# Performance work log

Hardware: AMD Instinct MI355X
Metric: run time of the kernel (lower is better)

The kernel has to match this reference:

```python
import jax, jax.numpy as jnp
import numpy as np

B, T, S0 = 8, 4, 4096
D_MODEL, H, D, R, RANK = 2048, 16, 128, 64, 512
C = D - R  # content dim = 64


def _rope(x, positions):
    # x: [B, H, T, R]; rotate-half style RoPE as in the torch module
    half = x.shape[-1] // 2
    inv_freq = 1.0 / (10000.0 ** (jnp.arange(half, dtype=jnp.float32) / half))
    freqs = positions.astype(jnp.float32)[:, None] * inv_freq[None, :]  # [T, half]
    cos = jnp.cos(freqs)[None, None].astype(x.dtype)
    sin = jnp.sin(freqs)[None, None].astype(x.dtype)
    x1, x2 = x[..., :half], x[..., half:]
    return jnp.concatenate([x1 * cos - x2 * sin, x1 * sin + x2 * cos], axis=-1)


def setup_inputs() -> dict:
    key = jax.random.key(0)
    ks = jax.random.split(key, 9)
    s = 0.02
    return {
        "x": jax.random.normal(ks[0], (B, T, D_MODEL), jnp.float32),
        "cache_c_kv": jax.random.normal(ks[1], (B, S0, RANK), jnp.float32),
        "cache_k_rope": jax.random.normal(ks[2], (B, S0, H, R), jnp.float32),
        "w_q": jax.random.normal(ks[3], (D_MODEL, H * C), jnp.float32) * s,
        "w_q_rope": jax.random.normal(ks[4], (D_MODEL, H * R), jnp.float32) * s,
        "w_kv_down": jax.random.normal(ks[5], (D_MODEL, RANK), jnp.float32) * s,
        "w_kv_up": jax.random.normal(ks[6], (RANK, H * D), jnp.float32) * s,
        "w_k_rope": jax.random.normal(ks[7], (D_MODEL, H * R), jnp.float32) * s,
        "w_out": jax.random.normal(ks[8], (H * D, D_MODEL), jnp.float32) * s,
    }


def reference(x, cache_c_kv, cache_k_rope, w_q, w_q_rope, w_kv_down, w_kv_up, w_k_rope, w_out):
    cache_len = cache_c_kv.shape[1]
    positions = jnp.arange(cache_len, cache_len + T)

    # queries
    q_content = (x @ w_q).reshape(B, T, H, C).transpose(0, 2, 1, 3)        # [B,H,T,C]
    q_rope = (x @ w_q_rope).reshape(B, T, H, R).transpose(0, 2, 1, 3)      # [B,H,T,R]
    q_rope = _rope(q_rope, positions)
    q = jnp.concatenate([q_content, q_rope], axis=-1)                       # [B,H,T,D]

    # new compressed kv + rope keys, append to cache
    c_kv_new = x @ w_kv_down                                                # [B,T,RANK]
    k_rope_new = (x @ w_k_rope).reshape(B, T, H, R).transpose(0, 2, 1, 3)
    k_rope_new = _rope(k_rope_new, positions).transpose(0, 2, 1, 3)         # [B,T,H,R]
    c_kv = jnp.concatenate([cache_c_kv, c_kv_new], axis=1)                  # [B,S,RANK]
    k_rope = jnp.concatenate([cache_k_rope, k_rope_new], axis=1)            # [B,S,H,R]

    # decompress full cache every step (the expensive MLA pattern)
    S = c_kv.shape[1]
    kv = (c_kv @ w_kv_up).reshape(B, S, H, D)                               # [B,S,H,D]
    k_content = kv[..., :C].transpose(0, 2, 1, 3)                           # [B,H,S,C]
    v = kv.transpose(0, 2, 1, 3)                                            # [B,H,S,D]
    k = jnp.concatenate([k_content, k_rope.transpose(0, 2, 1, 3)], axis=-1) # [B,H,S,D]

    # kv_cache present => is_prefill False => no causal mask (faithful to source)
    scale = 1.0 / jnp.sqrt(jnp.asarray(D, dtype=q.dtype))
    scores = jnp.einsum('bhtd,bhsd->bhts', q, k) * scale
    attn = jax.nn.softmax(scores, axis=-1)
    out = jnp.einsum('bhts,bhsd->bhtd', attn, v)                            # [B,H,T,D]
    out = out.transpose(0, 2, 1, 3).reshape(B, T, H * D)
    return out @ w_out                                                       # [B,T,D_MODEL]
```

## Files before the change

kernel.cpp:

```cpp
#include <hip/hip_runtime.h>
#include <hip/hip_fp16.h>
#include <cmath>

#define BB 8
#define TT 4
#define HH 16
#define DDIM 128
#define RRDIM 64
#define CCDIM 64
#define RANKC 512
#define DMODEL 2048
#define S0C 4096
#define NQ 64
#define HD 2048
#define NACT 3584
#define NSC 65
#define NG 17
#define SPAD 4160
#define SCALE_ATT 0.08838834764831845f
#define LP 72

typedef __attribute__((ext_vector_type(8))) short bf16x8;
typedef __attribute__((ext_vector_type(4))) float f32x4;
typedef unsigned short ushortT;

#define AIDX(row, kk) ((row)*132 + (((row)>>2)<<2) + (kk))

static __device__ __forceinline__ unsigned short f2bf(float x) {
  unsigned u = __float_as_uint(x);
  u += 0x7FFFu + ((u >> 16) & 1u);
  return (unsigned short)(u >> 16);
}
static __device__ __forceinline__ float bf2f(unsigned v16) {
  return __uint_as_float(v16 << 16);
}
static __device__ __forceinline__ unsigned pk2(float a, float b) {
  return (unsigned)f2bf(a) | ((unsigned)f2bf(b) << 16);
}

__global__ __launch_bounds__(256) void k_front(const float* __restrict__ A,
                                               const float* __restrict__ w0,
                                               const float* __restrict__ w1,
                                               const float* __restrict__ w2,
                                               const float* __restrict__ w3,
                                               const float* __restrict__ cckv,
                                               float* __restrict__ part,
                                               ushortT* __restrict__ ckvT) {
  __shared__ float shf[4352];
  const int tid = threadIdx.x;
  const int bx = blockIdx.x;
  if (bx < 448) {
    const int cb = bx % 28;
    const int k0 = (bx / 28) * 128;
    const float* W; int N, lc0, off;
    if (cb < 8)       { W = w0; N = 1024; lc0 = cb * 128;        off = 0; }
    else if (cb < 16) { W = w1; N = 1024; lc0 = (cb - 8) * 128;  off = 1024; }
    else if (cb < 20) { W = w2; N = 512;  lc0 = (cb - 16) * 128; off = 2048; }
    else              { W = w3; N = 1024; lc0 = (cb - 20) * 128; off = 2560; }
    {
      const int row = tid >> 3;
      const int kseg = (tid & 7) * 16;
      const float4* s4 = reinterpret_cast<const float4*>(A + (size_t)row * DMODEL + k0 + kseg);
      float4 v0 = s4[0], v1 = s4[1], v2 = s4[2], v3 = s4[3];
      *reinterpret_cast<float4*>(&shf[AIDX(row, kseg)])      = v0;
      *reinterpret_cast<float4*>(&shf[AIDX(row, kseg + 4)])  = v1;
      *reinterpret_cast<float4*>(&shf[AIDX(row, kseg + 8)])  = v2;
      *reinterpret_cast<float4*>(&shf[AIDX(row, kseg + 12)]) = v3;
    }
    __syncthreads();
    const int cg = tid & 31;
    const int rg = tid >> 5;
    float acc[4][4];
    #pragma unroll
    for (int r = 0; r < 4; ++r)
      #pragma unroll
      for (int c = 0; c < 4; ++c) acc[r][c] = 0.f;
    #pragma unroll 4
    for (int kk = 0; kk < 128; ++kk) {
      const float4 w4 = *reinterpret_cast<const float4*>(W + (size_t)(k0 + kk) * N + lc0 + cg * 4);
      const float wv[4] = {w4.x, w4.y, w4.z, w4.w};
      #pragma unroll
      for (int r = 0; r < 4; ++r) {
        const float av = shf[AIDX(rg * 4 + r, kk)];
        #pragma unroll
        for (int c = 0; c < 4; ++c) acc[r][c] = fmaf(av, wv[c], acc[r][c]);
      }
    }
    #pragma unroll
    for (int r = 0; r < 4; ++r) {
      float4 o = make_float4(acc[r][0], acc[r][1], acc[r][2], acc[r][3]);
      *reinterpret_cast<float4*>(part + ((size_t)(bx / 28) * 32 + rg * 4 + r) * NACT + off + lc0 + cg * 4) = o;
    }
  } else if (bx < 960) {
    ushortT* tlds = reinterpret_cast<ushortT*>(shf);
    const int idx = bx - 448;
    const int b = idx >> 6, c = idx & 63;
    const float* src = cckv + ((size_t)b * S0C + c * 64) * RANKC;
    ushortT* dstT = ckvT + ((size_t)(b * NSC + c) * RANKC) * 64;
    const int s = tid >> 2, rq = tid & 3;
    const int rloc = tid >> 1, shalf = (tid & 1) * 32;
    for (int slab = 0; slab < 4; ++slab) {
      const int r0 = slab * 128;
      #pragma unroll
      for (int i = 0; i < 8; ++i) {
        const float4 v = *reinterpret_cast<const float4*>(src + (size_t)s * RANKC + r0 + rq * 32 + i * 4);
        *reinterpret_cast<uint2*>(&tlds[s * 136 + rq * 32 + i * 4]) =
            make_uint2(pk2(v.x, v.y), pk2(v.z, v.w));
      }
      __syncthreads();
      unsigned wv[16];
      #pragma unroll
      for (int k = 0; k < 16; ++k) {
        const unsigned t0 = tlds[(shalf + 2 * k)     * 136 + rloc];
        const unsigned t1 = tlds[(shalf + 2 * k + 1) * 136 + rloc];
        wv[k] = t0 | (t1 << 16);
      }
      uint4* d = reinterpret_cast<uint4*>(dstT + ((size_t)(r0 + rloc)) * 64 + shalf);
      d[0] = make_uint4(wv[0], wv[1], wv[2], wv[3]);
      d[1] = make_uint4(wv[4], wv[5], wv[6], wv[7]);
      d[2] = make_uint4(wv[8], wv[9], wv[10], wv[11]);
      d[3] = make_uint4(wv[12], wv[13], wv[14], wv[15]);
      __syncthreads();
    }
  } else {
    const int b = bx - 960;
    uint4* p = reinterpret_cast<uint4*>(ckvT + ((size_t)(b * NSC + 64) * RANKC) * 64);
    const uint4 z = make_uint4(0, 0, 0, 0);
    for (int i = tid; i < 4096; i += 256) p[i] = z;
  }
}

__global__ __launch_bounds__(256) void k_proj(const float* __restrict__ A,
                                              const float* __restrict__ W,
                                              float* __restrict__ part,
                                              int N, int NTOT, int coloff) {
  __shared__ float a_lds[4352];
  const int tid = threadIdx.x;
  const int c0 = blockIdx.x * 128;
  const int k0 = blockIdx.y * 128;
  {
    const int row = tid >> 3;
    const int kseg = (tid & 7) * 16;
    const float4* s4 = reinterpret_cast<const float4*>(A + (size_t)row * DMODEL + k0 + kseg);
    float4 v0 = s4[0], v1 = s4[1], v2 = s4[2], v3 = s4[3];
    *reinterpret_cast<float4*>(&a_lds[AIDX(row, kseg)])      = v0;
    *reinterpret_cast<float4*>(&a_lds[AIDX(row, kseg + 4)])  = v1;
    *reinterpret_cast<float4*>(&a_lds[AIDX(row, kseg + 8)])  = v2;
    *reinterpret_cast<float4*>(&a_lds[AIDX(row, kseg + 12)]) = v3;
  }
  __syncthreads();
  const int cg = tid & 31;
  const int rg = tid >> 5;
  float acc[4][4];
  #pragma unroll
  for (int r = 0; r < 4; ++r)
    #pragma unroll
    for (int c = 0; c < 4; ++c) acc[r][c] = 0.f;
  #pragma unroll 4
  for (int kk = 0; kk < 128; ++kk) {
    const float4 w4 = *reinterpret_cast<const float4*>(W + (size_t)(k0 + kk) * N + c0 + cg * 4);
    const float wv[4] = {w4.x, w4.y, w4.z, w4.w};
    #pragma unroll
    for (int r = 0; r < 4; ++r) {
      const float av = a_lds[AIDX(rg * 4 + r, kk)];
      #pragma unroll
      for (int c = 0; c < 4; ++c) acc[r][c] = fmaf(av, wv[c], acc[r][c]);
    }
  }
  #pragma unroll
  for (int r = 0; r < 4; ++r) {
    float4 o = make_float4(acc[r][0], acc[r][1], acc[r][2], acc[r][3]);
    *reinterpret_cast<float4*>(part + ((size_t)blockIdx.y * 32 + rg * 4 + r) * NTOT + coloff + c0 + cg * 4) = o;
  }
}

__global__ __launch_bounds__(256) void k_reduce(const float* __restrict__ part,
                                                float* __restrict__ out, int total, int nsplit) {
  int g = blockIdx.x * 256 + threadIdx.x;
  if (g >= total) return;
  float s = 0.f;
  #pragma unroll 4
  for (int c = 0; c < nsplit; ++c) s += part[(size_t)c * total + g];
  out[g] = s;
}

__global__ __launch_bounds__(256) void k_qlatrope(const float* __restrict__ act,
                                                  const float* __restrict__ wup,
                                                  ushortT* __restrict__ qlat,
                                                  float* __restrict__ qrope,
                                                  float* __restrict__ ckvn,
                                                  float* __restrict__ krn,
                                                  ushortT* __restrict__ ckvT) {
  __shared__ float wt[64 * 132];
  __shared__ float a_s[32 * 68];
  const int tid = threadIdx.x;
  const int bx = blockIdx.x;
  if (bx < 64) {
    const int h = bx & 15;
    const int r0 = (bx >> 4) * 128;
    {
      const int r = tid >> 1;
      const int cseg = (tid & 1) * 32;
      const float* src = wup + (size_t)(r0 + r) * HD + h * DDIM + cseg;
      #pragma unroll
      for (int u = 0; u < 8; ++u) {
        const float4 v = *reinterpret_cast<const float4*>(src + u * 4);
        wt[(cseg + u * 4 + 0) * 132 + r] = v.x;
        wt[(cseg + u * 4 + 1) * 132 + r] = v.y;
        wt[(cseg + u * 4 + 2) * 132 + r] = v.z;
        wt[(cseg + u * 4 + 3) * 132 + r] = v.w;
      }
    }
    {
      const int bt = tid >> 3;
      const int cseg = (tid & 7) * 8;
      const float4* s4 = reinterpret_cast<const float4*>(act + (size_t)bt * NACT + h * CCDIM + cseg);
      float4 v0 = s4[0], v1 = s4[1];
      *reinterpret_cast<float4*>(&a_s[bt * 68 + cseg])     = v0;
      *reinterpret_cast<float4*>(&a_s[bt * 68 + cseg + 4]) = v1;
    }
    __syncthreads();
    const int r = tid & 127;
    const int bth = tid >> 7;
    float acc[16];
    #pragma unroll
    for (int i = 0; i < 16; ++i) acc[i] = 0.f;
    #pragma unroll 8
    for (int c = 0; c < 64; ++c) {
      const float wv = wt[c * 132 + r];
      #pragma unroll
      for (int i = 0; i < 16; ++i)
        acc[i] = fmaf(a_s[(bth * 16 + i) * 68 + c], wv, acc[i]);
    }
    #pragma unroll
    for (int i = 0; i < 16; ++i) {
      const int bt = bth * 16 + i;
      const int b = bt >> 2, t = bt & 3;
      qlat[((size_t)(b * NQ) + h * TT + t) * RANKC + r0 + r] = f2bf(acc[i]);
    }
    return;
  }
  int g = (bx - 64) * 256 + tid;
  if (g < BB * TT * HH * 32) {
    const int hj = g & 31;
    const int h = (g >> 5) & 15;
    const int t = (g >> 9) & 3;
    const int b = g >> 11;
    const float* arow = act + (size_t)(b * TT + t) * NACT + 1024 + h * RRDIM;
    const float x1 = arow[hj], x2 = arow[hj + 32];
    const double fr = (double)(S0C + t) * pow(10000.0, -(double)hj / 32.0);
    const float cs = (float)cos(fr), sn = (float)sin(fr);
    const int qi = h * TT + t;
    qrope[((size_t)b * NQ + qi) * RRDIM + hj]      = x1 * cs - x2 * sn;
    qrope[((size_t)b * NQ + qi) * RRDIM + hj + 32] = x1 * sn + x2 * cs;
    return;
  }
  g -= BB * TT * HH * 32;
  if (g < BB * TT * HH * 32) {
    const int hj = g & 31;
    const int h = (g >> 5) & 15;
    const int t = (g >> 9) & 3;
    const int b = g >> 11;
    const float* arow = act + (size_t)(b * TT + t) * NACT + 2560 + h * RRDIM;
    const float x1 = arow[hj], x2 = arow[hj + 32];
    const double fr = (double)(S0C + t) * pow(10000.0, -(double)hj / 32.0);
    const float cs = (float)cos(fr), sn = (float)sin(fr);
    krn[((size_t)(b * TT + t) * HH + h) * RRDIM + hj]      = x1 * cs - x2 * sn;
    krn[((size_t)(b * TT + t) * HH + h) * RRDIM + hj + 32] = x1 * sn + x2 * cs;
    return;
  }
  g -= BB * TT * HH * 32;
  if (g < BB * TT * RANKC) {
    const int r = g & 511;
    const int bt = g >> 9;
    const int b = bt >> 2, t = bt & 3;
    const float v = act[(size_t)bt * NACT + 2048 + r];
    ckvn[g] = v;
    ckvT[(((size_t)(b * NSC + 64) * RANKC) + r) * 64 + t] = f2bf(v);
  }
}

__global__ __launch_bounds__(256) void k_rscore(const float* __restrict__ cache_kr,
                                                const float* __restrict__ krn,
                                                const float* __restrict__ qrope,
                                                __half* __restrict__ rs) {
  const int bh = blockIdx.x;
  const int b = bh >> 4, h = bh & 15;
  const int tid = threadIdx.x;
  const int ql = tid & 3;
  float4 qf[4][4];
  const float* qrb = qrope + ((size_t)b * NQ + h * TT) * RRDIM;
  #pragma unroll
  for (int t = 0; t < 4; ++t)
    #pragma unroll
    for (int u = 0; u < 4; ++u)
      qf[t][u] = *reinterpret_cast<const float4*>(qrb + t * RRDIM + ql * 16 + u * 4);
  const int s0 = blockIdx.y * 512;
  #pragma unroll 1
  for (int pass = 0; pass < 8; ++pass) {
    const int s = s0 + pass * 64 + (tid >> 2);
    if (s < 4100) {
      const float* krow = (s < S0C)
        ? cache_kr + (((size_t)b * S0C + s) * HH + h) * RRDIM
        : krn + (((size_t)b * TT + (s - S0C)) * HH + h) * RRDIM;
      float p[4] = {0.f, 0.f, 0.f, 0.f};
      #pragma unroll
      for (int u = 0; u < 4; ++u) {
        const float4 kv = *reinterpret_cast<const float4*>(krow + ql * 16 + u * 4);
        #pragma unroll
        for (int t = 0; t < 4; ++t) {
          p[t] += kv.x * qf[t][u].x + kv.y * qf[t][u].y
                + kv.z * qf[t][u].z + kv.w * qf[t][u].w;
        }
      }
      #pragma unroll
      for (int t = 0; t < 4; ++t) {
        p[t] += __shfl_xor(p[t], 1, 4);
        p[t] += __shfl_xor(p[t], 2, 4);
      }
      rs[((size_t)bh * 4 + ql) * SPAD + s] = __float2half(p[ql] * SCALE_ATT);
    }
  }
}

__global__ __launch_bounds__(256) void k_score(
    const float* __restrict__ cckv, const float* __restrict__ ckvn,
    const ushortT* __restrict__ qlat, const __half* __restrict__ rs,
    float* __restrict__ ml, ushortT* __restrict__ Pg) {
  __shared__ ushortT smem[23040];
  ushortT* const QA0 = smem;
  ushortT* const QA1 = smem + 4608;
  ushortT* const KB0 = smem + 9216;
  ushortT* const KB1 = smem + 13824;
  ushortT* const PL  = smem + 18432;
  const int tid = threadIdx.x;
  const int lane = tid & 63;
  const int wv = tid >> 6;
  const int m0 = wv * 16;
  const int lm = lane & 15;
  const int lg = lane >> 4;
  const int b = blockIdx.x, chunk = blockIdx.y;
  const int scnt = (chunk < 64) ? 64 : TT;
  const float* bsrc = (chunk < 64)
      ? cckv + ((size_t)b * S0C + (size_t)chunk * 64) * RANKC
      : ckvn + (size_t)b * TT * RANKC;
  const ushortT* qsrc = qlat + (size_t)b * NQ * RANKC;

  const int srow = tid >> 2;
  const int rseg = (tid & 3) * 16;
  uint4 qreg[2];
  float4 kreg[4];
  auto loadA = [&](int kt) {
    const uint4* qp = reinterpret_cast<const uint4*>(qsrc + (size_t)srow * RANKC + kt * 64 + rseg);
    qreg[0] = qp[0]; qreg[1] = qp[1];
    if (srow < scnt) {
      const float4* kp = reinterpret_cast<const float4*>(bsrc + (size_t)srow * RANKC + kt * 64 + rseg);
      kreg[0] = kp[0]; kreg[1] = kp[1]; kreg[2] = kp[2]; kreg[3] = kp[3];
    } else {
      kreg[0] = make_float4(0.f, 0.f, 0.f, 0.f); kreg[1] = kreg[0]; kreg[2] = kreg[0]; kreg[3] = kreg[0];
    }
  };
  auto writeA = [&](ushortT* qa, ushortT* kb) {
    *reinterpret_cast<uint4*>(&qa[srow * LP + rseg])     = qreg[0];
    *reinterpret_cast<uint4*>(&qa[srow * LP + rseg + 8]) = qreg[1];
    *reinterpret_cast<uint4*>(&kb[srow * LP + rseg]) =
        make_uint4(pk2(kreg[0].x, kreg[0].y), pk2(kreg[0].z, kreg[0].w),
                   pk2(kreg[1].x, kreg[1].y), pk2(kreg[1].z, kreg[1].w));
    *reinterpret_cast<uint4*>(&kb[srow * LP + rseg + 8]) =
        make_uint4(pk2(kreg[2].x, kreg[2].y), pk2(kreg[2].z, kreg[2].w),
                   pk2(kreg[3].x, kreg[3].y), pk2(kreg[3].z, kreg[3].w));
  };

  f32x4 acc[4];
  #pragma unroll
  for (int st = 0; st < 4; ++st) acc[st] = (f32x4){0.f, 0.f, 0.f, 0.f};

  loadA(0);
  writeA(QA0, KB0);
  loadA(1);
  __syncthreads();
  for (int kt = 0; kt < 8; ++kt) {
    if (kt < 7) {
      writeA((kt & 1) ? QA0 : QA1, (kt & 1) ? KB0 : KB1);
      if (kt < 6) loadA(kt + 2);
    }
    const ushortT* qa = (kt & 1) ? QA1 : QA0;
    const ushortT* kb = (kt & 1) ? KB1 : KB0;
    #pragma unroll
    for (int ks = 0; ks < 2; ++ks) {
      const bf16x8 af = *reinterpret_cast<const bf16x8*>(&qa[(m0 + lm) * LP + ks * 32 + lg * 8]);
      #pragma unroll
      for (int st = 0; st < 4; ++st) {
        const bf16x8 bfv = *reinterpret_cast<const bf16x8*>(&kb[(st * 16 + lm) * LP + ks * 32 + lg * 8]);
        acc[st] = __builtin_amdgcn_mfma_f32_16x16x32_bf16(af, bfv, acc[st], 0, 0, 0);
      }
    }
    __syncthreads();
  }

  #pragma unroll
  for (int reg = 0; reg < 4; ++reg) {
    const int q = m0 + lg * 4 + reg;
    const __half* rp = rs + ((size_t)(b * HH + (q >> 2)) * TT + (q & 3)) * SPAD + chunk * 64;
    float vv[4];
    float mx = -1e30f;
    #pragma unroll
    for (int st = 0; st < 4; ++st) {
      const int sl = st * 16 + lm;
      const float val = (sl < scnt)
          ? fmaf(acc[st][reg], SCALE_ATT, __half2float(rp[st * 16 + lm]))
          : -1e30f;
      vv[st] = val;
      mx = fmaxf(mx, val);
    }
    #pragma unroll
    for (int off = 1; off < 16; off <<= 1) mx = fmaxf(mx, __shfl_xor(mx, off, 16));
    float sum = 0.f;
    #pragma unroll
    for (int st = 0; st < 4; ++st) {
      const float p = __expf(vv[st] - mx);
      vv[st] = p;
      sum += p;
    }
    #pragma unroll
    for (int off = 1; off < 16; off <<= 1) sum += __shfl_xor(sum, off, 16);
    #pragma unroll
    for (int st = 0; st < 4; ++st)
      PL[q * LP + st * 16 + lm] = f2bf(vv[st]);
    if (lm == 0) {
      const size_t mb = (((size_t)b * NSC + chunk) * NQ + q) * 2;
      ml[mb] = mx; ml[mb + 1] = sum;
    }
  }
  __syncthreads();

  {
    const int prow = tid >> 2;
    const int pseg = (tid & 3) * 16;
    const uint4* sp = reinterpret_cast<const uint4*>(&PL[prow * LP + pseg]);
    uint4* dp = reinterpret_cast<uint4*>(Pg + ((size_t)(b * NSC + chunk) * NQ + prow) * 64 + pseg);
    dp[0] = sp[0]; dp[1] = sp[1];
  }
}

__global__ __launch_bounds__(256) void k_pv(
    const ushortT* __restrict__ ckvT, const ushortT* __restrict__ Pg,
    const float* __restrict__ ml, float* __restrict__ olat,
    float* __restrict__ mlg) {
  __shared__ ushortT CT[128 * LP];
  __shared__ ushortT PLs[64 * LP];
  __shared__ float wlds[4][68];
  const int tid = threadIdx.x;
  const int lane = tid & 63;
  const int wv = tid >> 6;
  const int m0 = wv * 16;
  const int lm = lane & 15;
  const int lg = lane >> 4;
  const int b = blockIdx.x, g = blockIdx.y, rg = blockIdx.z;
  const int nc = (g < 16) ? 4 : 1;
  const int c0 = (g < 16) ? g * 4 : 64;

  if (lm == 0) {
    #pragma unroll
    for (int reg = 0; reg < 4; ++reg) {
      const int q = m0 + lg * 4 + reg;
      float mg = -1e30f;
      for (int c = 0; c < nc; ++c)
        mg = fmaxf(mg, ml[(((size_t)b * NSC + c0 + c) * NQ + q) * 2]);
      float la = 0.f;
      for (int c = 0; c < nc; ++c) {
        const size_t mb = (((size_t)b * NSC + c0 + c) * NQ + q) * 2;
        const float w = __expf(ml[mb] - mg);
        la = fmaf(ml[mb + 1], w, la);
        wlds[c][q] = w;
      }
      if (blockIdx.z == 0) {
        const size_t gb = (((size_t)b * NG + g) * NQ + q) * 2;
        mlg[gb] = mg; mlg[gb + 1] = la;
      }
    }
  }

  const int rloc = tid >> 1;
  const int shalf = (tid & 1) * 32;
  const int prow = tid >> 2;
  const int pseg = (tid & 3) * 16;
  uint4 ctreg[4];
  uint4 plreg[2];
  auto loadc = [&](int c) {
    const uint4* cp = reinterpret_cast<const uint4*>(
        ckvT + (((size_t)(b * NSC + c0 + c) * RANKC) + rg * 128 + rloc) * 64 + shalf);
    ctreg[0] = cp[0]; ctreg[1] = cp[1]; ctreg[2] = cp[2]; ctreg[3] = cp[3];
    const uint4* pp = reinterpret_cast<const uint4*>(
        Pg + ((size_t)(b * NSC + c0 + c) * NQ + prow) * 64 + pseg);
    plreg[0] = pp[0]; plreg[1] = pp[1];
  };
  auto writec = [&]() {
    uint4* d = reinterpret_cast<uint4*>(&CT[rloc * LP + shalf]);
    d[0] = ctreg[0]; d[1] = ctreg[1]; d[2] = ctreg[2]; d[3] = ctreg[3];
    uint4* p = reinterpret_cast<uint4*>(&PLs[prow * LP + pseg]);
    p[0] = plreg[0]; p[1] = plreg[1];
  };

  f32x4 OACC[8];
  #pragma unroll
  for (int nt = 0; nt < 8; ++nt) OACC[nt] = (f32x4){0.f, 0.f, 0.f, 0.f};

  loadc(0);
  __syncthreads();
  for (int c = 0; c < nc; ++c) {
    writec();
    __syncthreads();
    if (c + 1 < nc) loadc(c + 1);
    const bf16x8 pa0 = *reinterpret_cast<const bf16x8*>(&PLs[(m0 + lm) * LP + lg * 8]);
    const bf16x8 pa1 = *reinterpret_cast<const bf16x8*>(&PLs[(m0 + lm) * LP + 32 + lg * 8]);
    f32x4 a2[8];
    #pragma unroll
    for (int nt = 0; nt < 8; ++nt) a2[nt] = (f32x4){0.f, 0.f, 0.f, 0.f};
    #pragma unroll
    for (int nt = 0; nt < 8; ++nt) {
      const bf16x8 b0 = *reinterpret_cast<const bf16x8*>(&CT[(nt * 16 + lm) * LP + lg * 8]);
      const bf16x8 b1 = *reinterpret_cast<const bf16x8*>(&CT[(nt * 16 + lm) * LP + 32 + lg * 8]);
      a2[nt] = __builtin_amdgcn_mfma_f32_16x16x32_bf16(pa0, b0, a2[nt], 0, 0, 0);
      a2[nt] = __builtin_amdgcn_mfma_f32_16x16x32_bf16(pa1, b1, a2[nt], 0, 0, 0);
    }
    const f32x4 w = (f32x4){wlds[c][m0 + lg * 4 + 0], wlds[c][m0 + lg * 4 + 1],
                            wlds[c][m0 + lg * 4 + 2], wlds[c][m0 + lg * 4 + 3]};
    #pragma unroll
    for (int nt = 0; nt < 8; ++nt) OACC[nt] += w * a2[nt];
    __syncthreads();
  }

  const size_t obase = ((size_t)(b * NG + g) * NQ) * RANKC;
  #pragma unroll
  for (int nt = 0; nt < 8; ++nt)
    #pragma unroll
    for (int reg = 0; reg < 4; ++reg)
      olat[obase + (size_t)(m0 + lg * 4 + reg) * RANKC + rg * 128 + nt * 16 + lm] = OACC[nt][reg];
}

__global__ __launch_bounds__(512) void k_combF(const float* __restrict__ mlg,
                                               const float* __restrict__ olat,
                                               const float* __restrict__ wup,
                                               float* __restrict__ ohead) {
  __shared__ float wrow[4][20];
  __shared__ float att_lds[4][516];
  const int h = blockIdx.x, b = blockIdx.y;
  const int tid = threadIdx.x;
  const int wave = tid >> 6;
  const int i = wave >> 1;
  const int rhalf = wave & 1;
  const int rl = tid & 63;
  const int qi = h * TT + i;
  float m1 = -1e30f, l1 = 0.f;
  if (rl < NG) {
    const size_t base = (((size_t)b * NG + rl) * NQ + qi) * 2;
    m1 = mlg[base]; l1 = mlg[base + 1];
  }
  float M = m1;
  #pragma unroll
  for (int off = 1; off < 64; off <<= 1) M = fmaxf(M, __shfl_xor(M, off));
  float L = (rl < NG) ? l1 * __expf(m1 - M) : 0.f;
  #pragma unroll
  for (int off = 1; off < 64; off <<= 1) L += __shfl_xor(L, off);
  const float invL = 1.0f / L;
  if (rl < NG) wrow[i][rl] = __expf(m1 - M) * invL;
  __syncthreads();
  const int r0 = rhalf * 256 + rl * 4;
  float o0 = 0.f, o1 = 0.f, o2 = 0.f, o3 = 0.f;
  for (int c = 0; c < NG; ++c) {
    const float w = wrow[i][c];
    const float4 v = *reinterpret_cast<const float4*>(
        olat + (((size_t)b * NG + c) * NQ + qi) * RANKC + r0);
    o0 = fmaf(v.x, w, o0); o1 = fmaf(v.y, w, o1);
    o2 = fmaf(v.z, w, o2); o3 = fmaf(v.w, w, o3);
  }
  *reinterpret_cast<float4*>(&att_lds[i][r0]) = make_float4(o0, o1, o2, o3);
  __syncthreads();
  const int col = tid & 127;
  const int t = tid >> 7;
  float acc = 0.f;
  #pragma unroll 8
  for (int r = 0; r < RANKC; ++r)
    acc = fmaf(att_lds[t][r], wup[(size_t)r * HD + h * DDIM + col], acc);
  ohead[(size_t)(b * TT + t) * HD + h * DDIM + col] = acc;
}

extern "C" void kernel_launch(void* const* d_in, const int* in_sizes, int n_in,
                              void* d_out, int out_size, void* d_ws, size_t ws_size,
                              hipStream_t stream) {
  const float* x     = (const float*)d_in[0];
  const float* cckv  = (const float*)d_in[1];
  const float* ckr   = (const float*)d_in[2];
  const float* w_q   = (const float*)d_in[3];
  const float* w_qr  = (const float*)d_in[4];
  const float* w_kvd = (const float*)d_in[5];
  const float* w_kvu = (const float*)d_in[6];
  const float* w_kr  = (const float*)d_in[7];
  const float* w_out = (const float*)d_in[8];
  float* out = (float*)d_out;
  float* ws = (float*)d_ws;

  size_t off = 0;
  float* act      = ws + off; off += 32ull * NACT;
  ushortT* qlat   = (ushortT*)(ws + off); off += 131072;
  float* qrope    = ws + off; off += 32768;
  float* ckvn     = ws + off; off += 16384;
  float* krn      = ws + off; off += 32768;
  float* mlb      = ws + off; off += (size_t)BB * NSC * NQ * 2;
  float* mlgb     = ws + off; off += (size_t)BB * NG * NQ * 2;
  float* ohead    = ws + off; off += 65536;
  __half* rsb     = (__half*)(ws + off); off += 1064960;
  ushortT* ckvT   = (ushortT*)(ws + off); off += 8519680;
  ushortT* Pgb    = (ushortT*)(ws + off); off += 1064960;
  float* regB  = ws + off;
  float* part0 = regB;
  float* olat  = regB;
  float* part3 = regB;

  k_front<<<dim3(968), 256, 0, stream>>>(x, w_q, w_qr, w_kvd, w_kr, cckv, part0, ckvT);
  k_reduce<<<dim3(448), 256, 0, stream>>>(part0, act, 32 * NACT, 16);
  k_qlatrope<<<dim3(256), 256, 0, stream>>>(act, w_kvu, qlat, qrope, ckvn, krn, ckvT);
  k_rscore<<<dim3(128, 9), 256, 0, stream>>>(ckr, krn, qrope, rsb);

  k_score<<<dim3(BB, NSC), 256, 0, stream>>>(cckv, ckvn, qlat, rsb, mlb, Pgb);
  k_pv<<<dim3(BB, NG, 4), 256, 0, stream>>>(ckvT, Pgb, mlb, olat, mlgb);

  k_combF<<<dim3(16, 8), 512, 0, stream>>>(mlgb, olat, w_kvu, ohead);
  k_proj<<<dim3(16, 16), 256, 0, stream>>>(ohead, w_out, part3, 2048, 2048, 0);
  k_reduce<<<dim3(256), 256, 0, stream>>>(part3, out, 32 * HD, 16);
}
```

Baseline: 235.8 us.

## Pre-convert latent cache to bf16 row layout and drop LDS staging in score/PV

k_front now also writes a bf16 row-major copy of the compressed KV cache, plus a zeroed padding chunk. k_score reads MFMA operands from that copy directly out of global memory, with queries held in registers, instead of converting fp32 through double-buffered LDS. k_score and k_pv are split into 128-thread blocks over query halves, and k_pv computes its softmax-merge weights with wave shuffles instead of LDS. This removes the repeated fp32 reads, conversions and barriers in the hot kernels. The cost is an extra bf16 cache write in the front kernel and uncoalesced-ish global operand loads with no LDS reuse.

```diff
diff --git a/kernel.cpp b/kernel.cpp
--- a/kernel.cpp
+++ b/kernel.cpp
@@ -18,7 +18,6 @@
 #define NG 17
 #define SPAD 4160
 #define SCALE_ATT 0.08838834764831845f
-#define LP 72
 
 typedef __attribute__((ext_vector_type(8))) short bf16x8;
 typedef __attribute__((ext_vector_type(4))) float f32x4;
@@ -30,9 +29,6 @@
   unsigned u = __float_as_uint(x);
   u += 0x7FFFu + ((u >> 16) & 1u);
   return (unsigned short)(u >> 16);
-}
-static __device__ __forceinline__ float bf2f(unsigned v16) {
-  return __uint_as_float(v16 << 16);
 }
 static __device__ __forceinline__ unsigned pk2(float a, float b) {
   return (unsigned)f2bf(a) | ((unsigned)f2bf(b) << 16);
@@ -45,6 +41,7 @@
                                                const float* __restrict__ w3,
                                                const float* __restrict__ cckv,
                                                float* __restrict__ part,
+                                               ushortT* __restrict__ ckvB,
                                                ushortT* __restrict__ ckvT) {
   __shared__ float shf[4352];
   const int tid = threadIdx.x;
@@ -96,6 +93,7 @@
     const int idx = bx - 448;
     const int b = idx >> 6, c = idx & 63;
     const float* src = cckv + ((size_t)b * S0C + c * 64) * RANKC;
+    ushortT* dstB = ckvB + ((size_t)(b * NSC + c) * 64) * RANKC;
     ushortT* dstT = ckvT + ((size_t)(b * NSC + c) * RANKC) * 64;
     const int s = tid >> 2, rq = tid & 3;
     const int rloc = tid >> 1, shalf = (tid & 1) * 32;
@@ -104,26 +102,32 @@
       #pragma unroll
       for (int i = 0; i < 8; ++i) {
         const float4 v = *reinterpret_cast<const float4*>(src + (size_t)s * RANKC + r0 + rq * 32 + i * 4);
-        *reinterpret_cast<uint2*>(&tlds[s * 136 + rq * 32 + i * 4]) =
-            make_uint2(pk2(v.x, v.y), pk2(v.z, v.w));
+        const uint2 pk = make_uint2(pk2(v.x, v.y), pk2(v.z, v.w));
+        *reinterpret_cast<uint2*>(&tlds[s * 136 + rq * 32 + i * 4]) = pk;
+        *reinterpret_cast<uint2*>(&dstB[(size_t)s * RANKC + r0 + rq * 32 + i * 4]) = pk;
       }
       __syncthreads();
-      unsigned wv[16];
+      unsigned pkv[16];
       #pragma unroll
       for (int k = 0; k < 16; ++k) {
         const unsigned t0 = tlds[(shalf + 2 * k)     * 136 + rloc];
         const unsigned t1 = tlds[(shalf + 2 * k + 1) * 136 + rloc];
-        wv[k] = t0 | (t1 << 16);
+        pkv[k] = t0 | (t1 << 16);
       }
       uint4* d = reinterpret_cast<uint4*>(dstT + ((size_t)(r0 + rloc)) * 64 + shalf);
-      d[0] = make_uint4(wv[0], wv[1], wv[2], wv[3]);
-      d[1] = make_uint4(wv[4], wv[5], wv[6], wv[7]);
-      d[2] = make_uint4(wv[8], wv[9], wv[10], wv[11]);
-      d[3] = make_uint4(wv[12], wv[13], wv[14], wv[15]);
+      d[0] = make_uint4(pkv[0], pkv[1], pkv[2], pkv[3]);
+      d[1] = make_uint4(pkv[4], pkv[5], pkv[6], pkv[7]);
+      d[2] = make_uint4(pkv[8], pkv[9], pkv[10], pkv[11]);
+      d[3] = make_uint4(pkv[12], pkv[13], pkv[14], pkv[15]);
       __syncthreads();
     }
+  } else if (bx < 968) {
+    const int b = bx - 960;
+    uint4* p = reinterpret_cast<uint4*>(ckvB + ((size_t)(b * NSC + 64) * 64) * RANKC);
+    const uint4 z = make_uint4(0, 0, 0, 0);
+    for (int i = tid; i < 4096; i += 256) p[i] = z;
   } else {
-    const int b = bx - 960;
+    const int b = bx - 968;
     uint4* p = reinterpret_cast<uint4*>(ckvT + ((size_t)(b * NSC + 64) * RANKC) * 64);
     const uint4 z = make_uint4(0, 0, 0, 0);
     for (int i = tid; i < 4096; i += 256) p[i] = z;
@@ -188,8 +192,8 @@
                                                   const float* __restrict__ wup,
                                                   ushortT* __restrict__ qlat,
                                                   float* __restrict__ qrope,
-                                                  float* __restrict__ ckvn,
                                                   float* __restrict__ krn,
+                                                  ushortT* __restrict__ ckvB,
                                                   ushortT* __restrict__ ckvT) {
   __shared__ float wt[64 * 132];
   __shared__ float a_s[32 * 68];
@@ -274,9 +278,9 @@
     const int r = g & 511;
     const int bt = g >> 9;
     const int b = bt >> 2, t = bt & 3;
-    const float v = act[(size_t)bt * NACT + 2048 + r];
-    ckvn[g] = v;
-    ckvT[(((size_t)(b * NSC + 64) * RANKC) + r) * 64 + t] = f2bf(v);
+    const ushortT bv = f2bf(act[(size_t)bt * NACT + 2048 + r]);
+    ckvB[(((size_t)(b * NSC + 64) * 64) + t) * RANKC + r] = bv;
+    ckvT[(((size_t)(b * NSC + 64) * RANKC) + r) * 64 + t] = bv;
   }
 }
 
@@ -323,94 +327,52 @@
   }
 }
 
-__global__ __launch_bounds__(256) void k_score(
-    const float* __restrict__ cckv, const float* __restrict__ ckvn,
-    const ushortT* __restrict__ qlat, const __half* __restrict__ rs,
-    float* __restrict__ ml, ushortT* __restrict__ Pg) {
-  __shared__ ushortT smem[23040];
-  ushortT* const QA0 = smem;
-  ushortT* const QA1 = smem + 4608;
-  ushortT* const KB0 = smem + 9216;
-  ushortT* const KB1 = smem + 13824;
-  ushortT* const PL  = smem + 18432;
-  const int tid = threadIdx.x;
+__global__ __launch_bounds__(128) void k_score(
+    const ushortT* __restrict__ ckvB, const ushortT* __restrict__ qlat,
+    const __half* __restrict__ rs, float* __restrict__ ml,
+    ushortT* __restrict__ Pg) {
+  __shared__ ushortT PL[2][16 * 72];
+  const int tid = threadIdx.x;
+  const int wv = tid >> 6;
   const int lane = tid & 63;
-  const int wv = tid >> 6;
-  const int m0 = wv * 16;
-  const int lm = lane & 15;
-  const int lg = lane >> 4;
+  const int lm = lane & 15, lg = lane >> 4;
   const int b = blockIdx.x, chunk = blockIdx.y;
+  const int qbase = blockIdx.z * 32 + wv * 16;
   const int scnt = (chunk < 64) ? 64 : TT;
-  const float* bsrc = (chunk < 64)
-      ? cckv + ((size_t)b * S0C + (size_t)chunk * 64) * RANKC
-      : ckvn + (size_t)b * TT * RANKC;
-  const ushortT* qsrc = qlat + (size_t)b * NQ * RANKC;
-
-  const int srow = tid >> 2;
-  const int rseg = (tid & 3) * 16;
-  uint4 qreg[2];
-  float4 kreg[4];
-  auto loadA = [&](int kt) {
-    const uint4* qp = reinterpret_cast<const uint4*>(qsrc + (size_t)srow * RANKC + kt * 64 + rseg);
-    qreg[0] = qp[0]; qreg[1] = qp[1];
-    if (srow < scnt) {
-      const float4* kp = reinterpret_cast<const float4*>(bsrc + (size_t)srow * RANKC + kt * 64 + rseg);
-      kreg[0] = kp[0]; kreg[1] = kp[1]; kreg[2] = kp[2]; kreg[3] = kp[3];
-    } else {
-      kreg[0] = make_float4(0.f, 0.f, 0.f, 0.f); kreg[1] = kreg[0]; kreg[2] = kreg[0]; kreg[3] = kreg[0];
-    }
-  };
-  auto writeA = [&](ushortT* qa, ushortT* kb) {
-    *reinterpret_cast<uint4*>(&qa[srow * LP + rseg])     = qreg[0];
-    *reinterpret_cast<uint4*>(&qa[srow * LP + rseg + 8]) = qreg[1];
-    *reinterpret_cast<uint4*>(&kb[srow * LP + rseg]) =
-        make_uint4(pk2(kreg[0].x, kreg[0].y), pk2(kreg[0].z, kreg[0].w),
-                   pk2(kreg[1].x, kreg[1].y), pk2(kreg[1].z, kreg[1].w));
-    *reinterpret_cast<uint4*>(&kb[srow * LP + rseg + 8]) =
-        make_uint4(pk2(kreg[2].x, kreg[2].y), pk2(kreg[2].z, kreg[2].w),
-                   pk2(kreg[3].x, kreg[3].y), pk2(kreg[3].z, kreg[3].w));
-  };
-
+
+  const ushortT* qrow = qlat + ((size_t)b * NQ + qbase + lm) * RANKC + lg * 8;
+  bf16x8 qa[16];
+  #pragma unroll
+  for (int ks = 0; ks < 16; ++ks)
+    qa[ks] = *reinterpret_cast<const bf16x8*>(qrow + ks * 32);
+
+  const ushortT* bbase = ckvB + ((size_t)(b * NSC + chunk) * 64) * RANKC;
   f32x4 acc[4];
   #pragma unroll
   for (int st = 0; st < 4; ++st) acc[st] = (f32x4){0.f, 0.f, 0.f, 0.f};
-
-  loadA(0);
-  writeA(QA0, KB0);
-  loadA(1);
-  __syncthreads();
-  for (int kt = 0; kt < 8; ++kt) {
-    if (kt < 7) {
-      writeA((kt & 1) ? QA0 : QA1, (kt & 1) ? KB0 : KB1);
-      if (kt < 6) loadA(kt + 2);
-    }
-    const ushortT* qa = (kt & 1) ? QA1 : QA0;
-    const ushortT* kb = (kt & 1) ? KB1 : KB0;
-    #pragma unroll
-    for (int ks = 0; ks < 2; ++ks) {
-      const bf16x8 af = *reinterpret_cast<const bf16x8*>(&qa[(m0 + lm) * LP + ks * 32 + lg * 8]);
-      #pragma unroll
-      for (int st = 0; st < 4; ++st) {
-        const bf16x8 bfv = *reinterpret_cast<const bf16x8*>(&kb[(st * 16 + lm) * LP + ks * 32 + lg * 8]);
-        acc[st] = __builtin_amdgcn_mfma_f32_16x16x32_bf16(af, bfv, acc[st], 0, 0, 0);
-      }
-    }
-    __syncthreads();
+  #pragma unroll
+  for (int ks = 0; ks < 16; ++ks) {
+    #pragma unroll
+    for (int st = 0; st < 4; ++st) {
+      const bf16x8 bf = *reinterpret_cast<const bf16x8*>(
+          bbase + (size_t)(st * 16 + lm) * RANKC + ks * 32 + lg * 8);
+      acc[st] = __builtin_amdgcn_mfma_f32_16x16x32_bf16(qa[ks], bf, acc[st], 0, 0, 0);
+    }
   }
 
   #pragma unroll
   for (int reg = 0; reg < 4; ++reg) {
-    const int q = m0 + lg * 4 + reg;
-    const __half* rp = rs + ((size_t)(b * HH + (q >> 2)) * TT + (q & 3)) * SPAD + chunk * 64;
-    float vv[4];
+    const int qi = qbase + lg * 4 + reg;
+    const __half* rp = rs + (((size_t)(b * HH) + (qi >> 2)) * TT + (qi & 3)) * SPAD + chunk * 64;
+    float vvv[4];
     float mx = -1e30f;
     #pragma unroll
     for (int st = 0; st < 4; ++st) {
       const int sl = st * 16 + lm;
       const float val = (sl < scnt)
-          ? fmaf(acc[st][reg], SCALE_ATT, __half2float(rp[st * 16 + lm]))
+          ? fmaf(acc[st][reg], SCALE_ATT, __half2float(rp[sl]))
           : -1e30f;
-      vv[st] = val;
+      vvv[st] = val;
       mx = fmaxf(mx, val);
     }
     #pragma unroll
@@ -418,117 +380,88 @@
     float sum = 0.f;
     #pragma unroll
     for (int st = 0; st < 4; ++st) {
-      const float p = __expf(vv[st] - mx);
-      vv[st] = p;
+      const float p = __expf(vvv[st] - mx);
+      vvv[st] = p;
       sum += p;
     }
     #pragma unroll
     for (int off = 1; off < 16; off <<= 1) sum += __shfl_xor(sum, off, 16);
     #pragma unroll
     for (int st = 0; st < 4; ++st)
-      PL[q * LP + st * 16 + lm] = f2bf(vv[st]);
+      PL[wv][(lg * 4 + reg) * 72 + st * 16 + lm] = f2bf(vvv[st]);
     if (lm == 0) {
-      const size_t mb = (((size_t)b * NSC + chunk) * NQ + q) * 2;
+      const size_t mb = (((size_t)b * NSC + chunk) * NQ + qi) * 2;
       ml[mb] = mx; ml[mb + 1] = sum;
     }
   }
   __syncthreads();
-
   {
-    const int prow = tid >> 2;
-    const int pseg = (tid & 3) * 16;
-    const uint4* sp = reinterpret_cast<const uint4*>(&PL[prow * LP + pseg]);
-    uint4* dp = reinterpret_cast<uint4*>(Pg + ((size_t)(b * NSC + chunk) * NQ + prow) * 64 + pseg);
+    const int row = lane >> 2, seg = (lane & 3) * 16;
+    const uint4* sp = reinterpret_cast<const uint4*>(&PL[wv][row * 72 + seg]);
+    uint4* dp = reinterpret_cast<uint4*>(
+        Pg + ((size_t)(b * NSC + chunk) * NQ + qbase + row) * 64 + seg);
     dp[0] = sp[0]; dp[1] = sp[1];
   }
 }
 
-__global__ __launch_bounds__(256) void k_pv(
+__global__ __launch_bounds__(128) void k_pv(
     const ushortT* __restrict__ ckvT, const ushortT* __restrict__ Pg,
     const float* __restrict__ ml, float* __restrict__ olat,
     float* __restrict__ mlg) {
-  __shared__ ushortT CT[128 * LP];
-  __shared__ ushortT PLs[64 * LP];
-  __shared__ float wlds[4][68];
-  const int tid = threadIdx.x;
+  const int tid = threadIdx.x;
+  const int wv = tid >> 6;
   const int lane = tid & 63;
-  const int wv = tid >> 6;
-  const int m0 = wv * 16;
-  const int lm = lane & 15;
-  const int lg = lane >> 4;
-  const int b = blockIdx.x, g = blockIdx.y, rg = blockIdx.z;
+  const int lm = lane & 15, lg = lane >> 4;
+  const int b = blockIdx.x, g = blockIdx.y;
+  const int rg = blockIdx.z >> 1, qh = blockIdx.z & 1;
+  const int qbase = qh * 32 + wv * 16;
   const int nc = (g < 16) ? 4 : 1;
   const int c0 = (g < 16) ? g * 4 : 64;
 
-  if (lm == 0) {
-    #pragma unroll
-    for (int reg = 0; reg < 4; ++reg) {
-      const int q = m0 + lg * 4 + reg;
-      float mg = -1e30f;
-      for (int c = 0; c < nc; ++c)
-        mg = fmaxf(mg, ml[(((size_t)b * NSC + c0 + c) * NQ + q) * 2]);
-      float la = 0.f;
-      for (int c = 0; c < nc; ++c) {
-        const size_t mb = (((size_t)b * NSC + c0 + c) * NQ + q) * 2;
-        const float w = __expf(ml[mb] - mg);
-        la = fmaf(ml[mb + 1], w, la);
-        wlds[c][q] = w;
-      }
-      if (blockIdx.z == 0) {
-        const size_t gb = (((size_t)b * NG + g) * NQ + q) * 2;
-        mlg[gb] = mg; mlg[gb + 1] = la;
-      }
-    }
-  }
-
-  const int rloc = tid >> 1;
-  const int shalf = (tid & 1) * 32;
-  const int prow = tid >> 2;
-  const int pseg = (tid & 3) * 16;
-  uint4 ctreg[4];
-  uint4 plreg[2];
-  auto loadc = [&](int c) {
-    const uint4* cp = reinterpret_cast<const uint4*>(
-        ckvT + (((size_t)(b * NSC + c0 + c) * RANKC) + rg * 128 + rloc) * 64 + shalf);
-    ctreg[0] = cp[0]; ctreg[1] = cp[1]; ctreg[2] = cp[2]; ctreg[3] = cp[3];
-    const uint4* pp = reinterpret_cast<const uint4*>(
-        Pg + ((size_t)(b * NSC + c0 + c) * NQ + prow) * 64 + pseg);
-    plreg[0] = pp[0]; plreg[1] = pp[1];
-  };
-  auto writec = [&]() {
-    uint4* d = reinterpret_cast<uint4*>(&CT[rloc * LP + shalf]);
-    d[0] = ctreg[0]; d[1] = ctreg[1]; d[2] = ctreg[2]; d[3] = ctreg[3];
-    uint4* p = reinterpret_cast<uint4*>(&PLs[prow * LP + pseg]);
-    p[0] = plreg[0]; p[1] = plreg[1];
-  };
+  float m_cl = -1e30f, l_cl = 0.f;
+  if (lg < nc) {
+    const size_t mb = (((size_t)b * NSC + c0 + lg) * NQ + qbase + lm) * 2;
+    m_cl = ml[mb]; l_cl = ml[mb + 1];
+  }
+  float mg = fmaxf(m_cl, __shfl_xor(m_cl, 16));
+  mg = fmaxf(mg, __shfl_xor(mg, 32));
+  const float wgt = (lg < nc) ? __expf(m_cl - mg) : 0.f;
+  float la = l_cl * wgt;
+  la += __shfl_xor(la, 16);
+  la += __shfl_xor(la, 32);
+  if (rg == 0 && lg == 0) {
+    const size_t gb = (((size_t)b * NG + g) * NQ + qbase + lm) * 2;
+    mlg[gb] = mg; mlg[gb + 1] = la;
+  }
+  float wf[4][4];
+  #pragma unroll
+  for (int c = 0; c < 4; ++c)
+    #pragma unroll
+    for (int reg = 0; reg < 4; ++reg)
+      wf[c][reg] = __shfl(wgt, c * 16 + lg * 4 + reg);
 
   f32x4 OACC[8];
   #pragma unroll
   for (int nt = 0; nt < 8; ++nt) OACC[nt] = (f32x4){0.f, 0.f, 0.f, 0.f};
 
-  loadc(0);
-  __syncthreads();
   for (int c = 0; c < nc; ++c) {
-    writec();
-    __syncthreads();
-    if (c + 1 < nc) loadc(c + 1);
-    const bf16x8 pa0 = *reinterpret_cast<const bf16x8*>(&PLs[(m0 + lm) * LP + lg * 8]);
-    const bf16x8 pa1 = *reinterpret_cast<const bf16x8*>(&PLs[(m0 + lm) * LP + 32 + lg * 8]);
+    const ushortT* pb = Pg + ((size_t)(b * NSC + c0 + c) * NQ + qbase + lm) * 64 + lg * 8;
+    const bf16x8 pa0 = *reinterpret_cast<const bf16x8*>(pb);
+    const bf16x8 pa1 = *reinterpret_cast<const bf16x8*>(pb + 32);
+    const ushortT* vb = ckvT + (((size_t)(b * NSC + c0 + c) * RANKC) + rg * 128 + lm) * 64 + lg * 8;
     f32x4 a2[8];
     #pragma unroll
     for (int nt = 0; nt < 8; ++nt) a2[nt] = (f32x4){0.f, 0.f, 0.f, 0.f};
     #pragma unroll
     for (int nt = 0; nt < 8; ++nt) {
-      const bf16x8 b0 = *reinterpret_cast<const bf16x8*>(&CT[(nt * 16 + lm) * LP + lg * 8]);
-      const bf16x8 b1 = *reinterpret_cast<const bf16x8*>(&CT[(nt * 16 + lm) * LP + 32 + lg * 8]);
+      const bf16x8 b0 = *reinterpret_cast<const bf16x8*>(vb + (size_t)nt * 16 * 64);
+      const bf16x8 b1 = *reinterpret_cast<const bf16x8*>(vb + (size_t)nt * 16 * 64 + 32);
       a2[nt] = __builtin_amdgcn_mfma_f32_16x16x32_bf16(pa0, b0, a2[nt], 0, 0, 0);
       a2[nt] = __builtin_amdgcn_mfma_f32_16x16x32_bf16(pa1, b1, a2[nt], 0, 0, 0);
     }
-    const f32x4 w = (f32x4){wlds[c][m0 + lg * 4 + 0], wlds[c][m0 + lg * 4 + 1],
-                            wlds[c][m0 + lg * 4 + 2], wlds[c][m0 + lg * 4 + 3]};
-    #pragma unroll
-    for (int nt = 0; nt < 8; ++nt) OACC[nt] += w * a2[nt];
-    __syncthreads();
+    const f32x4 wv4 = {wf[c][0], wf[c][1], wf[c][2], wf[c][3]};
+    #pragma unroll
+    for (int nt = 0; nt < 8; ++nt) OACC[nt] += wv4 * a2[nt];
   }
 
   const size_t obase = ((size_t)(b * NG + g) * NQ) * RANKC;
@@ -536,7 +469,7 @@
   for (int nt = 0; nt < 8; ++nt)
     #pragma unroll
     for (int reg = 0; reg < 4; ++reg)
-      olat[obase + (size_t)(m0 + lg * 4 + reg) * RANKC + rg * 128 + nt * 16 + lm] = OACC[nt][reg];
+      olat[obase + (size_t)(qbase + lg * 4 + reg) * RANKC + rg * 128 + nt * 16 + lm] = OACC[nt][reg];
 }
 
 __global__ __launch_bounds__(512) void k_combF(const float* __restrict__ mlg,
@@ -605,12 +538,12 @@
   float* act      = ws + off; off += 32ull * NACT;
   ushortT* qlat   = (ushortT*)(ws + off); off += 131072;
   float* qrope    = ws + off; off += 32768;
-  float* ckvn     = ws + off; off += 16384;
   float* krn      = ws + off; off += 32768;
   float* mlb      = ws + off; off += (size_t)BB * NSC * NQ * 2;
   float* mlgb     = ws + off; off += (size_t)BB * NG * NQ * 2;
   float* ohead    = ws + off; off += 65536;
   __half* rsb     = (__half*)(ws + off); off += 1064960;
+  ushortT* ckvB   = (ushortT*)(ws + off); off += 8519680;
   ushortT* ckvT   = (ushortT*)(ws + off); off += 8519680;
   ushortT* Pgb    = (ushortT*)(ws + off); off += 1064960;
   float* regB  = ws + off;
@@ -618,13 +551,13 @@
   float* olat  = regB;
   float* part3 = regB;
 
-  k_front<<<dim3(968), 256, 0, stream>>>(x, w_q, w_qr, w_kvd, w_kr, cckv, part0, ckvT);
+  k_front<<<dim3(976), 256, 0, stream>>>(x, w_q, w_qr, w_kvd, w_kr, cckv, part0, ckvB, ckvT);
   k_reduce<<<dim3(448), 256, 0, stream>>>(part0, act, 32 * NACT, 16);
-  k_qlatrope<<<dim3(256), 256, 0, stream>>>(act, w_kvu, qlat, qrope, ckvn, krn, ckvT);
+  k_qlatrope<<<dim3(256), 256, 0, stream>>>(act, w_kvu, qlat, qrope, krn, ckvB, ckvT);
   k_rscore<<<dim3(128, 9), 256, 0, stream>>>(ckr, krn, qrope, rsb);
 
-  k_score<<<dim3(BB, NSC), 256, 0, stream>>>(cckv, ckvn, qlat, rsb, mlb, Pgb);
-  k_pv<<<dim3(BB, NG, 4), 256, 0, stream>>>(ckvT, Pgb, mlb, olat, mlgb);
+  k_score<<<dim3(BB, NSC, 2), 128, 0, stream>>>(ckvB, qlat, rsb, mlb, Pgb);
+  k_pv<<<dim3(BB, NG, 8), 128, 0, stream>>>(ckvT, Pgb, mlb, olat, mlgb);
 
   k_combF<<<dim3(16, 8), 512, 0, stream>>>(mlgb, olat, w_kvu, ohead);
   k_proj<<<dim3(16, 16), 256, 0, stream>>>(ohead, w_out, part3, 2048, 2048, 0);
```

Result: faster. 213.0 us (-9.7%).
